# Kernel tuning notes

Hardware: AMD Instinct MI355X
Metric: run time of the kernel (lower is better)

## Reference

```python
import jax, jax.numpy as jnp
import numpy as np

TOP_K = 8
N_EXPERTS = 64
ALPHA = 0.1
NORM_TOPK = True
SEQ_AUX = True


def setup_inputs() -> dict:
    key = jax.random.key(0)
    k1, k2 = jax.random.split(key)
    B, S, H = 4, 4096, 2048
    hidden_states = jax.random.normal(k1, (B, S, H), dtype=jnp.float32)
    # kaiming_uniform_(a=sqrt(5)) => bound = 1/sqrt(fan_in)
    bound = 1.0 / np.sqrt(H)
    weight = jax.random.uniform(k2, (N_EXPERTS, H), dtype=jnp.float32,
                                minval=-bound, maxval=bound)
    return {"hidden_states": hidden_states, "weight": weight}


def reference(hidden_states, weight):
    B, S, H = hidden_states.shape
    E, K = N_EXPERTS, TOP_K
    x = hidden_states.reshape(-1, H)                 # [T, H], T = B*S
    logits = jnp.einsum('th,eh->te', x, weight)      # gating GEMM
    scores = jax.nn.softmax(logits, axis=-1)         # [T, E]
    topk_weight, topk_idx = jax.lax.top_k(scores, K) # [T, K]
    if K > 1 and NORM_TOPK:
        topk_weight = topk_weight / (topk_weight.sum(-1, keepdims=True) + 1e-20)

    # batch-level load stats (bincount over selections)
    expert_loads = jnp.zeros((E,), jnp.float32).at[topk_idx.reshape(-1)].add(1.0)

    # sequence-level auxiliary load-balancing loss
    if SEQ_AUX:
        idx_b = topk_idx.reshape(B, S * K)           # [B, S*K]
        ce = jnp.zeros((B, E), jnp.float32)
        ce = ce.at[jnp.arange(B)[:, None], idx_b].add(1.0)
        ce = ce / (S * K / E)
        mean_scores = scores.reshape(B, S, E).mean(axis=1)   # [B, E]
        aux_loss = (ce * mean_scores).sum(axis=1).mean() * ALPHA
    else:
        ce = jax.nn.one_hot(topk_idx.reshape(-1), E).mean(0)
        Pi = scores.mean(0)
        aux_loss = (Pi * ce * E).sum() * ALPHA

    return (topk_idx, topk_weight, aux_loss, expert_loads)
```

## Files before the change

### kernel.cpp

```cpp
#include <hip/hip_runtime.h>
#include <hip/hip_bf16.h>
#include <math.h>

#define TOK 16384
#define HDIM 2048
#define NE 64
#define NB 4
#define KTOP 8
#define KC 64
#define NC (HDIM / KC)

typedef __attribute__((ext_vector_type(8))) __bf16 bf16x8;
typedef __attribute__((ext_vector_type(4))) float f32x4;
typedef unsigned int uint;

__device__ __forceinline__ uint asu(float f) { union { float f; uint u; } c; c.f = f; return c.u; }
__device__ __forceinline__ float asf(uint u) { union { uint u; float f; } c; c.u = u; return c.f; }

__device__ __forceinline__ void split3(float v, uint& h, uint& m, uint& l) {
  uint u = asu(v);
  h = u & 0xffff0000u;
  float d = v - asf(h);
  m = asu(d) & 0xffff0000u;
  float d2 = d - asf(m);
  l = asu(d2);
}

__device__ __forceinline__ void split8(float4 a, float4 b,
                                       bf16x8& h8, bf16x8& m8, bf16x8& l8) {
  union { uint4 u; bf16x8 v; } H, M, L;
  uint h0, m0, l0, h1, m1, l1;
  split3(a.x, h0, m0, l0); split3(a.y, h1, m1, l1);
  H.u.x = (h0 >> 16) | (h1 & 0xffff0000u);
  M.u.x = (m0 >> 16) | (m1 & 0xffff0000u);
  L.u.x = (l0 >> 16) | (l1 & 0xffff0000u);
  split3(a.z, h0, m0, l0); split3(a.w, h1, m1, l1);
  H.u.y = (h0 >> 16) | (h1 & 0xffff0000u);
  M.u.y = (m0 >> 16) | (m1 & 0xffff0000u);
  L.u.y = (l0 >> 16) | (l1 & 0xffff0000u);
  split3(b.x, h0, m0, l0); split3(b.y, h1, m1, l1);
  H.u.z = (h0 >> 16) | (h1 & 0xffff0000u);
  M.u.z = (m0 >> 16) | (m1 & 0xffff0000u);
  L.u.z = (l0 >> 16) | (l1 & 0xffff0000u);
  split3(b.z, h0, m0, l0); split3(b.w, h1, m1, l1);
  H.u.w = (h0 >> 16) | (h1 & 0xffff0000u);
  M.u.w = (m0 >> 16) | (m1 & 0xffff0000u);
  L.u.w = (l0 >> 16) | (l1 & 0xffff0000u);
  h8 = H.v; m8 = M.v; l8 = L.v;
}

__device__ __forceinline__ void gl_lds16(const void* g, void* l) {
  __builtin_amdgcn_global_load_lds(
      (const __attribute__((address_space(1))) void*)g,
      (__attribute__((address_space(3))) void*)l, 16, 0, 0);
}

__global__ __launch_bounds__(256) void wsplit(const float* __restrict__ w,
                                              char* __restrict__ wpk) {
  int t = blockIdx.x * 256 + threadIdx.x;
  int lane = t & 63;
  int f2 = (t >> 6) & 1, half = (t >> 7) & 1, ks = (t >> 8) & 1, c = t >> 9;
  int e = half * 32 + f2 * 16 + (lane & 15);
  int k = c * 64 + ks * 32 + ((lane >> 4) << 3);
  const float* p = w + (size_t)e * HDIM + k;
  bf16x8 h8, m8, l8;
  split8(*(const float4*)p, *(const float4*)(p + 4), h8, m8, l8);
  union { bf16x8 v; uint4 u; } H, M, L;
  H.v = h8; M.v = m8; L.v = l8;
  size_t base = ((size_t)c * 24 + (size_t)(((ks * 2 + half) * 2 + f2) * 3)) * 1024
                + (size_t)lane * 16;
  *(uint4*)(wpk + base) = H.u;
  *(uint4*)(wpk + base + 1024) = M.u;
  *(uint4*)(wpk + base + 2048) = L.u;
}

__global__ __launch_bounds__(512) void gate_fused(const float* __restrict__ x,
                                                  const char* __restrict__ wpk,
                                                  float* __restrict__ out,
                                                  float* __restrict__ ce,
                                                  float* __restrict__ ssum) {
  __shared__ __align__(16) char lds[49152];
  __shared__ float hist[NE];

  const int tid = threadIdx.x;
  const int bid = blockIdx.x;
  const int t0 = bid * 64;
  const int b = bid >> 6;
  const int lane = tid & 63;
  const int wid = tid >> 6;
  const int half = wid & 1;
  const int tg = (wid >> 1) << 4;

  if (tid < NE) hist[tid] = 0.f;

  char* buf0 = lds;
  char* buf1 = lds + 24576;

  const float* xrow = x + (size_t)(t0 + tg + (lane & 15)) * HDIM + ((lane >> 4) << 3);

  f32x4 acc[2] = {{0.f, 0.f, 0.f, 0.f}, {0.f, 0.f, 0.f, 0.f}};

  {
    const char* wsp0 = wpk + (size_t)lane * 16;
    gl_lds16(wsp0 + (0 * 8 + wid) * 1024, buf0 + (0 * 8 + wid) * 1024);
    gl_lds16(wsp0 + (1 * 8 + wid) * 1024, buf0 + (1 * 8 + wid) * 1024);
    gl_lds16(wsp0 + (2 * 8 + wid) * 1024, buf0 + (2 * 8 + wid) * 1024);
  }
  float4 xa0 = *(const float4*)(xrow);
  float4 xa1 = *(const float4*)(xrow + 4);
  float4 xa2 = *(const float4*)(xrow + 32);
  float4 xa3 = *(const float4*)(xrow + 36);
  float4 xb0 = *(const float4*)(xrow + 64);
  float4 xb1 = *(const float4*)(xrow + 68);
  float4 xb2 = *(const float4*)(xrow + 96);
  float4 xb3 = *(const float4*)(xrow + 100);
  asm volatile("s_waitcnt vmcnt(4)" ::: "memory");
  __builtin_amdgcn_s_barrier();
  asm volatile("" ::: "memory");

#define CHUNK(c, X0, X1, X2, X3, BR, BW)                                        \
  {                                                                             \
    if ((c) + 1 < NC) {                              \
      const char* wsp = wpk + (size_t)((c) + 1) * 24576 + (size_t)lane * 16;    \
      gl_lds16(wsp + (0 * 8 + wid) * 1024, BW + (0 * 8 + wid) * 1024);          \
      gl_lds16(wsp + (1 * 8 + wid) * 1024, BW + (1 * 8 + wid) * 1024);          \
      gl_lds16(wsp + (2 * 8 + wid) * 1024, BW + (2 * 8 + wid) * 1024);          \
    }                                                                           \
    bf16x8 ah0, am0, al0, ah1, am1, al1;                     \
    split8(X0, X1, ah0, am0, al0);                                              \
    split8(X2, X3, ah1, am1, al1);                                              \
    if ((c) + 2 < NC) {                                    \
      const float* xp = xrow + ((c) + 2) * 64;                                  \
      X0 = *(const float4*)(xp);                                                \
      X1 = *(const float4*)(xp + 4);                                            \
      X2 = *(const float4*)(xp + 32);                                           \
      X3 = *(const float4*)(xp + 36);                                           \
    }                                                                           \
    _Pragma("unroll")                                 \
    for (int f2 = 0; f2 < 2; ++f2) {                                            \
      const char* bb0 = BR + (size_t)(((0 * 2 + half) * 2 + f2) * 3) * 1024 + lane * 16; \
      bf16x8 bh = *(const bf16x8*)(bb0);                                        \
      bf16x8 bm = *(const bf16x8*)(bb0 + 1024);                                 \
      bf16x8 bl = *(const bf16x8*)(bb0 + 2048);                                 \
      acc[f2] = __builtin_amdgcn_mfma_f32_16x16x32_bf16(ah0, bh, acc[f2], 0, 0, 0); \
      acc[f2] = __builtin_amdgcn_mfma_f32_16x16x32_bf16(ah0, bm, acc[f2], 0, 0, 0); \
      acc[f2] = __builtin_amdgcn_mfma_f32_16x16x32_bf16(am0, bh, acc[f2], 0, 0, 0); \
      acc[f2] = __builtin_amdgcn_mfma_f32_16x16x32_bf16(ah0, bl, acc[f2], 0, 0, 0); \
      acc[f2] = __builtin_amdgcn_mfma_f32_16x16x32_bf16(al0, bh, acc[f2], 0, 0, 0); \
      acc[f2] = __builtin_amdgcn_mfma_f32_16x16x32_bf16(am0, bm, acc[f2], 0, 0, 0); \
      const char* bb1 = BR + (size_t)(((1 * 2 + half) * 2 + f2) * 3) * 1024 + lane * 16; \
      bf16x8 kh = *(const bf16x8*)(bb1);                                        \
      bf16x8 km = *(const bf16x8*)(bb1 + 1024);                                 \
      bf16x8 kl = *(const bf16x8*)(bb1 + 2048);                                 \
      acc[f2] = __builtin_amdgcn_mfma_f32_16x16x32_bf16(ah1, kh, acc[f2], 0, 0, 0); \
      acc[f2] = __builtin_amdgcn_mfma_f32_16x16x32_bf16(ah1, km, acc[f2], 0, 0, 0); \
      acc[f2] = __builtin_amdgcn_mfma_f32_16x16x32_bf16(am1, kh, acc[f2], 0, 0, 0); \
      acc[f2] = __builtin_amdgcn_mfma_f32_16x16x32_bf16(ah1, kl, acc[f2], 0, 0, 0); \
      acc[f2] = __builtin_amdgcn_mfma_f32_16x16x32_bf16(al1, kh, acc[f2], 0, 0, 0); \
      acc[f2] = __builtin_amdgcn_mfma_f32_16x16x32_bf16(am1, km, acc[f2], 0, 0, 0); \
    }                                                                           \
          \
    if ((c) < NC - 2) { asm volatile("s_waitcnt vmcnt(4)" ::: "memory"); }      \
    else              { asm volatile("s_waitcnt vmcnt(0)" ::: "memory"); }      \
    __builtin_amdgcn_s_barrier();                                               \
    asm volatile("" ::: "memory");                                              \
  }

#pragma unroll 1
  for (int cc = 0; cc < NC; cc += 2) {
    CHUNK(cc,     xa0, xa1, xa2, xa3, buf0, buf1);
    CHUNK(cc + 1, xb0, xb1, xb2, xb3, buf1, buf0);
  }
#undef CHUNK

  float (*sc)[65] = (float(*)[65])lds;
#pragma unroll
  for (int f2 = 0; f2 < 2; ++f2) {
    int e = half * 32 + f2 * 16 + (lane & 15);
    int tk = tg + ((lane >> 4) << 2);
    sc[e][tk + 0] = acc[f2][0];
    sc[e][tk + 1] = acc[f2][1];
    sc[e][tk + 2] = acc[f2][2];
    sc[e][tk + 3] = acc[f2][3];
  }
  __syncthreads();

  const int t = tid >> 3;
  const int j = tid & 7;
  float p[8];
#pragma unroll
  for (int i = 0; i < 8; ++i) p[i] = sc[j * 8 + i][t];

  float m = p[0];
#pragma unroll
  for (int i = 1; i < 8; ++i) m = fmaxf(m, p[i]);
  m = fmaxf(m, __shfl_xor(m, 1, 8));
  m = fmaxf(m, __shfl_xor(m, 2, 8));
  m = fmaxf(m, __shfl_xor(m, 4, 8));
  float s = 0.f;
#pragma unroll
  for (int i = 0; i < 8; ++i) { p[i] = __expf(p[i] - m); s += p[i]; }
  s += __shfl_xor(s, 1, 8);
  s += __shfl_xor(s, 2, 8);
  s += __shfl_xor(s, 4, 8);
  float inv = 1.f / s;
#pragma unroll
  for (int i = 0; i < 8; ++i) { p[i] *= inv; sc[j * 8 + i][t] = p[i]; }

  unsigned used = 0;
  float wsum = 0.f;
  float wv[KTOP];
  int wi_[KTOP];
#pragma unroll
  for (int sel = 0; sel < KTOP; ++sel) {
    float bv = -1.f;
    int bi = 0;
#pragma unroll
    for (int i = 0; i < 8; ++i) {
      bool ok = !((used >> i) & 1u);
      if (ok && p[i] > bv) { bv = p[i]; bi = i; }
    }
    int ge = j * 8 + bi;
#pragma unroll
    for (int mk = 1; mk < 8; mk <<= 1) {
      float ov = __shfl_xor(bv, mk, 8);
      int og = __shfl_xor(ge, mk, 8);
      if (ov > bv || (ov == bv && og < ge)) { bv = ov; ge = og; }
    }
    if ((ge >> 3) == j) used |= 1u << (ge & 7);
    wv[sel] = bv;
    wi_[sel] = ge;
    wsum += bv;
  }
  if (j == 0) {
    float winv = 1.f / (wsum + 1e-20f);
#pragma unroll
    for (int sel = 0; sel < KTOP; ++sel) {
      out[(size_t)(t0 + t) * KTOP + sel] = (float)wi_[sel];
      out[(size_t)TOK * KTOP + (size_t)(t0 + t) * KTOP + sel] = wv[sel] * winv;
      atomicAdd(&hist[wi_[sel]], 1.f);
    }
  }
  __syncthreads();

  if (tid < NE) {
    float ssl = 0.f;
#pragma unroll
    for (int tt = 0; tt < 64; ++tt) ssl += sc[tid][tt];
    atomicAdd(&ssum[b * NE + tid], ssl);
    atomicAdd(&ce[b * NE + tid], hist[tid]);
  }
}

__global__ __launch_bounds__(64) void gate_final(const float* __restrict__ ce,
                                                 const float* __restrict__ ssum,
                                                 float* __restrict__ out) {
  const int e = threadIdx.x;
  float loads = 0.f, aux = 0.f;
#pragma unroll
  for (int b = 0; b < NB; ++b) {
    float c = ce[b * 64 + e];
    loads += c;
    aux += (c / 512.0f) * (ssum[b * 64 + e] / 4096.0f);
  }
  out[(size_t)2 * TOK * KTOP + 1 + e] = loads;
#pragma unroll
  for (int off = 32; off > 0; off >>= 1) aux += __shfl_down(aux, off);
  if (e == 0) out[(size_t)2 * TOK * KTOP] = aux * (0.1f / 4.0f);
}

extern "C" void kernel_launch(void* const* d_in, const int* in_sizes, int n_in,
                              void* d_out, int out_size, void* d_ws, size_t ws_size,
                              hipStream_t stream) {
  const float* x = (const float*)d_in[0];
  const float* w = (const float*)d_in[1];
  float* out = (float*)d_out;

  char* wpk = (char*)d_ws;
  float* ce = (float*)(wpk + (size_t)NC * 24576);
  float* ssum = ce + NB * NE;

  hipMemsetAsync(ce, 0, 2 * NB * NE * sizeof(float), stream);
  wsplit<<<dim3(64), dim3(256), 0, stream>>>(w, wpk);
  gate_fused<<<dim3(TOK / 64), dim3(512), 0, stream>>>(x, wpk, out, ce, ssum);
  gate_final<<<dim3(1), dim3(64), 0, stream>>>(ce, ssum, out);
}
```

Baseline: 60.72 us.

## Load packed weights straight to registers instead of staging through LDS

The GEMM main loop no longer stages the split bf16 weight chunks into double-buffered LDS with global_load_lds. Each wave now loads only its own half of the weights directly from global memory into register double buffers (WA/WB). This frees about 48KB of LDS and adds launch_bounds(512,2), which allows two blocks per CU. The hipMemsetAsync is folded into the wsplit kernel, and the explicit vmcnt waits are dropped. The costs are more register pressure from 24 uint4 buffers and redundant weight reads from L2 across the four token-group waves.

```diff
diff --git a/kernel.cpp b/kernel.cpp
--- a/kernel.cpp
+++ b/kernel.cpp
@@ -16,6 +16,7 @@
 
 __device__ __forceinline__ uint asu(float f) { union { float f; uint u; } c; c.f = f; return c.u; }
 __device__ __forceinline__ float asf(uint u) { union { uint u; float f; } c; c.u = u; return c.f; }
+__device__ __forceinline__ bf16x8 u2b(uint4 u) { union { uint4 u; bf16x8 b; } c; c.u = u; return c.b; }
 
 __device__ __forceinline__ void split3(float v, uint& h, uint& m, uint& l) {
   uint u = asu(v);
@@ -49,14 +50,12 @@
   h8 = H.v; m8 = M.v; l8 = L.v;
 }
 
-__device__ __forceinline__ void gl_lds16(const void* g, void* l) {
-  __builtin_amdgcn_global_load_lds(
-      (const __attribute__((address_space(1))) void*)g,
-      (__attribute__((address_space(3))) void*)l, 16, 0, 0);
-}
-
 __global__ __launch_bounds__(256) void wsplit(const float* __restrict__ w,
-                                              char* __restrict__ wpk) {
+                                              char* __restrict__ wpk,
+                                              float* __restrict__ stats) {
+  if (blockIdx.x == 0 && threadIdx.x < 128) {
+    *(float4*)(stats + threadIdx.x * 4) = make_float4(0.f, 0.f, 0.f, 0.f);
+  }
   int t = blockIdx.x * 256 + threadIdx.x;
   int lane = t & 63;
   int f2 = (t >> 6) & 1, half = (t >> 7) & 1, ks = (t >> 8) & 1, c = t >> 9;
@@ -67,19 +66,19 @@
   split8(*(const float4*)p, *(const float4*)(p + 4), h8, m8, l8);
   union { bf16x8 v; uint4 u; } H, M, L;
   H.v = h8; M.v = m8; L.v = l8;
-  size_t base = ((size_t)c * 24 + (size_t)(((ks * 2 + half) * 2 + f2) * 3)) * 1024
-                + (size_t)lane * 16;
+  size_t base = (size_t)c * 24576 + (size_t)ks * 12288 + (size_t)half * 6144
+              + (size_t)f2 * 3072 + (size_t)lane * 16;
   *(uint4*)(wpk + base) = H.u;
   *(uint4*)(wpk + base + 1024) = M.u;
   *(uint4*)(wpk + base + 2048) = L.u;
 }
 
-__global__ __launch_bounds__(512) void gate_fused(const float* __restrict__ x,
-                                                  const char* __restrict__ wpk,
-                                                  float* __restrict__ out,
-                                                  float* __restrict__ ce,
-                                                  float* __restrict__ ssum) {
-  __shared__ __align__(16) char lds[49152];
+__global__ __launch_bounds__(512, 2) void gate_fused(const float* __restrict__ x,
+                                                     const char* __restrict__ wpk,
+                                                     float* __restrict__ out,
+                                                     float* __restrict__ ce,
+                                                     float* __restrict__ ssum) {
+  __shared__ float sc[NE][65];
   __shared__ float hist[NE];
 
   const int tid = threadIdx.x;
@@ -93,87 +92,79 @@
 
   if (tid < NE) hist[tid] = 0.f;
 
-  char* buf0 = lds;
-  char* buf1 = lds + 24576;
-
   const float* xrow = x + (size_t)(t0 + tg + (lane & 15)) * HDIM + ((lane >> 4) << 3);
+  const char* wbase = wpk + half * 6144 + lane * 16;
 
   f32x4 acc[2] = {{0.f, 0.f, 0.f, 0.f}, {0.f, 0.f, 0.f, 0.f}};
-
-  {
-    const char* wsp0 = wpk + (size_t)lane * 16;
-    gl_lds16(wsp0 + (0 * 8 + wid) * 1024, buf0 + (0 * 8 + wid) * 1024);
-    gl_lds16(wsp0 + (1 * 8 + wid) * 1024, buf0 + (1 * 8 + wid) * 1024);
-    gl_lds16(wsp0 + (2 * 8 + wid) * 1024, buf0 + (2 * 8 + wid) * 1024);
-  }
-  float4 xa0 = *(const float4*)(xrow);
-  float4 xa1 = *(const float4*)(xrow + 4);
-  float4 xa2 = *(const float4*)(xrow + 32);
-  float4 xa3 = *(const float4*)(xrow + 36);
-  float4 xb0 = *(const float4*)(xrow + 64);
-  float4 xb1 = *(const float4*)(xrow + 68);
-  float4 xb2 = *(const float4*)(xrow + 96);
-  float4 xb3 = *(const float4*)(xrow + 100);
-  asm volatile("s_waitcnt vmcnt(4)" ::: "memory");
-  __builtin_amdgcn_s_barrier();
-  asm volatile("" ::: "memory");
-
-#define CHUNK(c, X0, X1, X2, X3, BR, BW)                                        \
-  {                                                                             \
-    if ((c) + 1 < NC) {                              \
-      const char* wsp = wpk + (size_t)((c) + 1) * 24576 + (size_t)lane * 16;    \
-      gl_lds16(wsp + (0 * 8 + wid) * 1024, BW + (0 * 8 + wid) * 1024);          \
-      gl_lds16(wsp + (1 * 8 + wid) * 1024, BW + (1 * 8 + wid) * 1024);          \
-      gl_lds16(wsp + (2 * 8 + wid) * 1024, BW + (2 * 8 + wid) * 1024);          \
-    }                                                                           \
-    bf16x8 ah0, am0, al0, ah1, am1, al1;                     \
-    split8(X0, X1, ah0, am0, al0);                                              \
-    split8(X2, X3, ah1, am1, al1);                                              \
-    if ((c) + 2 < NC) {                                    \
-      const float* xp = xrow + ((c) + 2) * 64;                                  \
-      X0 = *(const float4*)(xp);                                                \
-      X1 = *(const float4*)(xp + 4);                                            \
-      X2 = *(const float4*)(xp + 32);                                           \
-      X3 = *(const float4*)(xp + 36);                                           \
-    }                                                                           \
-    _Pragma("unroll")                                 \
-    for (int f2 = 0; f2 < 2; ++f2) {                                            \
-      const char* bb0 = BR + (size_t)(((0 * 2 + half) * 2 + f2) * 3) * 1024 + lane * 16; \
-      bf16x8 bh = *(const bf16x8*)(bb0);                                        \
-      bf16x8 bm = *(const bf16x8*)(bb0 + 1024);                                 \
-      bf16x8 bl = *(const bf16x8*)(bb0 + 2048);                                 \
-      acc[f2] = __builtin_amdgcn_mfma_f32_16x16x32_bf16(ah0, bh, acc[f2], 0, 0, 0); \
-      acc[f2] = __builtin_amdgcn_mfma_f32_16x16x32_bf16(ah0, bm, acc[f2], 0, 0, 0); \
-      acc[f2] = __builtin_amdgcn_mfma_f32_16x16x32_bf16(am0, bh, acc[f2], 0, 0, 0); \
-      acc[f2] = __builtin_amdgcn_mfma_f32_16x16x32_bf16(ah0, bl, acc[f2], 0, 0, 0); \
-      acc[f2] = __builtin_amdgcn_mfma_f32_16x16x32_bf16(al0, bh, acc[f2], 0, 0, 0); \
-      acc[f2] = __builtin_amdgcn_mfma_f32_16x16x32_bf16(am0, bm, acc[f2], 0, 0, 0); \
-      const char* bb1 = BR + (size_t)(((1 * 2 + half) * 2 + f2) * 3) * 1024 + lane * 16; \
-      bf16x8 kh = *(const bf16x8*)(bb1);                                        \
-      bf16x8 km = *(const bf16x8*)(bb1 + 1024);                                 \
-      bf16x8 kl = *(const bf16x8*)(bb1 + 2048);                                 \
-      acc[f2] = __builtin_amdgcn_mfma_f32_16x16x32_bf16(ah1, kh, acc[f2], 0, 0, 0); \
-      acc[f2] = __builtin_amdgcn_mfma_f32_16x16x32_bf16(ah1, km, acc[f2], 0, 0, 0); \
-      acc[f2] = __builtin_amdgcn_mfma_f32_16x16x32_bf16(am1, kh, acc[f2], 0, 0, 0); \
-      acc[f2] = __builtin_amdgcn_mfma_f32_16x16x32_bf16(ah1, kl, acc[f2], 0, 0, 0); \
-      acc[f2] = __builtin_amdgcn_mfma_f32_16x16x32_bf16(al1, kh, acc[f2], 0, 0, 0); \
-      acc[f2] = __builtin_amdgcn_mfma_f32_16x16x32_bf16(am1, km, acc[f2], 0, 0, 0); \
-    }                                                                           \
-          \
-    if ((c) < NC - 2) { asm volatile("s_waitcnt vmcnt(4)" ::: "memory"); }      \
-    else              { asm volatile("s_waitcnt vmcnt(0)" ::: "memory"); }      \
-    __builtin_amdgcn_s_barrier();                                               \
-    asm volatile("" ::: "memory");                                              \
-  }
+  uint4 WA[12], WB[12];
+  float4 xa0, xa1, xa2, xa3, xb0, xb1, xb2, xb3;
+
+#define LOADW(W, c)                                                           \
+  {                                                                           \
+    const char* wp_ = wbase + (size_t)(c) * 24576;                            \
+    _Pragma("unroll")                                                         \
+    for (int ks = 0; ks < 2; ++ks)                                            \
+      _Pragma("unroll")                                                       \
+      for (int f2 = 0; f2 < 2; ++f2)                                          \
+        _Pragma("unroll")                                                     \
+        for (int pl = 0; pl < 3; ++pl)                                        \
+          W[ks * 6 + f2 * 3 + pl] =                                           \
+              *(const uint4*)(wp_ + ks * 12288 + f2 * 3072 + pl * 1024);      \
+  }
+
+#define LOADX(V0, V1, V2, V3, c)                                              \
+  {                                                                           \
+    const float* xp_ = xrow + (size_t)(c) * 64;                               \
+    V0 = *(const float4*)(xp_);                                               \
+    V1 = *(const float4*)(xp_ + 4);                                           \
+    V2 = *(const float4*)(xp_ + 32);                                          \
+    V3 = *(const float4*)(xp_ + 36);                                          \
+  }
+
+#define BODY(W, WN, X0, X1, X2, X3, c)                                        \
+  {                                                                           \
+    if ((c) + 1 < NC) LOADW(WN, (c) + 1);                                     \
+    bf16x8 ah0, am0, al0, ah1, am1, al1;                                      \
+    split8(X0, X1, ah0, am0, al0);                                            \
+    split8(X2, X3, ah1, am1, al1);                                            \
+    if ((c) + 2 < NC) LOADX(X0, X1, X2, X3, (c) + 2);                         \
+    _Pragma("unroll")                                                         \
+    for (int f2 = 0; f2 < 2; ++f2) {                                          \
+      bf16x8 bh0 = u2b(W[f2 * 3 + 0]);                                        \
+      bf16x8 bm0 = u2b(W[f2 * 3 + 1]);                                        \
+      bf16x8 bl0 = u2b(W[f2 * 3 + 2]);                                        \
+      acc[f2] = __builtin_amdgcn_mfma_f32_16x16x32_bf16(ah0, bh0, acc[f2], 0, 0, 0); \
+      acc[f2] = __builtin_amdgcn_mfma_f32_16x16x32_bf16(ah0, bm0, acc[f2], 0, 0, 0); \
+      acc[f2] = __builtin_amdgcn_mfma_f32_16x16x32_bf16(am0, bh0, acc[f2], 0, 0, 0); \
+      acc[f2] = __builtin_amdgcn_mfma_f32_16x16x32_bf16(ah0, bl0, acc[f2], 0, 0, 0); \
+      acc[f2] = __builtin_amdgcn_mfma_f32_16x16x32_bf16(al0, bh0, acc[f2], 0, 0, 0); \
+      acc[f2] = __builtin_amdgcn_mfma_f32_16x16x32_bf16(am0, bm0, acc[f2], 0, 0, 0); \
+      bf16x8 bh1 = u2b(W[6 + f2 * 3 + 0]);                                    \
+      bf16x8 bm1 = u2b(W[6 + f2 * 3 + 1]);                                    \
+      bf16x8 bl1 = u2b(W[6 + f2 * 3 + 2]);                                    \
+      acc[f2] = __builtin_amdgcn_mfma_f32_16x16x32_bf16(ah1, bh1, acc[f2], 0, 0, 0); \
+      acc[f2] = __builtin_amdgcn_mfma_f32_16x16x32_bf16(ah1, bm1, acc[f2], 0, 0, 0); \
+      acc[f2] = __builtin_amdgcn_mfma_f32_16x16x32_bf16(am1, bh1, acc[f2], 0, 0, 0); \
+      acc[f2] = __builtin_amdgcn_mfma_f32_16x16x32_bf16(ah1, bl1, acc[f2], 0, 0, 0); \
+      acc[f2] = __builtin_amdgcn_mfma_f32_16x16x32_bf16(al1, bh1, acc[f2], 0, 0, 0); \
+      acc[f2] = __builtin_amdgcn_mfma_f32_16x16x32_bf16(am1, bm1, acc[f2], 0, 0, 0); \
+    }                                                                         \
+    __builtin_amdgcn_s_barrier();             \
+  }
+
+  LOADW(WA, 0);
+  LOADX(xa0, xa1, xa2, xa3, 0);
+  LOADX(xb0, xb1, xb2, xb3, 1);
 
 #pragma unroll 1
   for (int cc = 0; cc < NC; cc += 2) {
-    CHUNK(cc,     xa0, xa1, xa2, xa3, buf0, buf1);
-    CHUNK(cc + 1, xb0, xb1, xb2, xb3, buf1, buf0);
-  }
-#undef CHUNK
-
-  float (*sc)[65] = (float(*)[65])lds;
+    BODY(WA, WB, xa0, xa1, xa2, xa3, cc);
+    BODY(WB, WA, xb0, xb1, xb2, xb3, cc + 1);
+  }
+#undef BODY
+#undef LOADW
+#undef LOADX
+
 #pragma unroll
   for (int f2 = 0; f2 < 2; ++f2) {
     int e = half * 32 + f2 * 16 + (lane & 15);
@@ -280,8 +271,7 @@
   float* ce = (float*)(wpk + (size_t)NC * 24576);
   float* ssum = ce + NB * NE;
 
-  hipMemsetAsync(ce, 0, 2 * NB * NE * sizeof(float), stream);
-  wsplit<<<dim3(64), dim3(256), 0, stream>>>(w, wpk);
+  wsplit<<<dim3(64), dim3(256), 0, stream>>>(w, wpk, ce);
   gate_fused<<<dim3(TOK / 64), dim3(512), 0, stream>>>(x, wpk, out, ce, ssum);
   gate_final<<<dim3(1), dim3(64), 0, stream>>>(ce, ssum, out);
 }
```

Measured after the change: 73.52 us. +21.1%, slower.

## Halve gating block tile to 32 tokens and fold stats zeroing into wsplit

Applied to the files above, without the earlier changes.

The fused gating kernel now processes 32 tokens per block with 256 threads instead of 64 tokens with 512, doubling the grid and allowing two blocks per CU. Each wave now issues six 16-byte global-to-LDS loads per weight chunk instead of three, and the scratch-score stride and wait counts are adjusted to match. The separate memset of the load and score statistics is removed; the first wsplit block zeroes them instead, saving one launch. In exchange, every packed weight chunk is streamed from L2 twice as many times overall, and the per-block reduction and global atomics are doubled.

```diff
diff --git a/kernel.cpp b/kernel.cpp
--- a/kernel.cpp
+++ b/kernel.cpp
@@ -9,6 +9,7 @@
 #define KTOP 8
 #define KC 64
 #define NC (HDIM / KC)
+#define BT 32
 
 typedef __attribute__((ext_vector_type(8))) __bf16 bf16x8;
 typedef __attribute__((ext_vector_type(4))) float f32x4;
@@ -56,7 +57,11 @@
 }
 
 __global__ __launch_bounds__(256) void wsplit(const float* __restrict__ w,
-                                              char* __restrict__ wpk) {
+                                              char* __restrict__ wpk,
+                                              float* __restrict__ stats) {
+  if (blockIdx.x == 0 && threadIdx.x < 128) {
+    *(float4*)(stats + threadIdx.x * 4) = make_float4(0.f, 0.f, 0.f, 0.f);
+  }
   int t = blockIdx.x * 256 + threadIdx.x;
   int lane = t & 63;
   int f2 = (t >> 6) & 1, half = (t >> 7) & 1, ks = (t >> 8) & 1, c = t >> 9;
@@ -67,25 +72,25 @@
   split8(*(const float4*)p, *(const float4*)(p + 4), h8, m8, l8);
   union { bf16x8 v; uint4 u; } H, M, L;
   H.v = h8; M.v = m8; L.v = l8;
-  size_t base = ((size_t)c * 24 + (size_t)(((ks * 2 + half) * 2 + f2) * 3)) * 1024
-                + (size_t)lane * 16;
+  size_t base = (size_t)c * 24576 + (size_t)ks * 12288 + (size_t)half * 6144
+              + (size_t)f2 * 3072 + (size_t)lane * 16;
   *(uint4*)(wpk + base) = H.u;
   *(uint4*)(wpk + base + 1024) = M.u;
   *(uint4*)(wpk + base + 2048) = L.u;
 }
 
-__global__ __launch_bounds__(512) void gate_fused(const float* __restrict__ x,
-                                                  const char* __restrict__ wpk,
-                                                  float* __restrict__ out,
-                                                  float* __restrict__ ce,
-                                                  float* __restrict__ ssum) {
+__global__ __launch_bounds__(256, 2) void gate_fused(const float* __restrict__ x,
+                                                     const char* __restrict__ wpk,
+                                                     float* __restrict__ out,
+                                                     float* __restrict__ ce,
+                                                     float* __restrict__ ssum) {
   __shared__ __align__(16) char lds[49152];
   __shared__ float hist[NE];
 
   const int tid = threadIdx.x;
   const int bid = blockIdx.x;
-  const int t0 = bid * 64;
-  const int b = bid >> 6;
+  const int t0 = bid * BT;
+  const int b = bid >> 7;
   const int lane = tid & 63;
   const int wid = tid >> 6;
   const int half = wid & 1;
@@ -102,9 +107,9 @@
 
   {
     const char* wsp0 = wpk + (size_t)lane * 16;
-    gl_lds16(wsp0 + (0 * 8 + wid) * 1024, buf0 + (0 * 8 + wid) * 1024);
-    gl_lds16(wsp0 + (1 * 8 + wid) * 1024, buf0 + (1 * 8 + wid) * 1024);
-    gl_lds16(wsp0 + (2 * 8 + wid) * 1024, buf0 + (2 * 8 + wid) * 1024);
+#pragma unroll
+    for (int i = 0; i < 6; ++i)
+      gl_lds16(wsp0 + (i * 4 + wid) * 1024, buf0 + (i * 4 + wid) * 1024);
   }
   float4 xa0 = *(const float4*)(xrow);
   float4 xa1 = *(const float4*)(xrow + 4);
@@ -114,23 +119,23 @@
   float4 xb1 = *(const float4*)(xrow + 68);
   float4 xb2 = *(const float4*)(xrow + 96);
   float4 xb3 = *(const float4*)(xrow + 100);
-  asm volatile("s_waitcnt vmcnt(4)" ::: "memory");
+  asm volatile("s_waitcnt vmcnt(8)" ::: "memory");
   __builtin_amdgcn_s_barrier();
   asm volatile("" ::: "memory");
 
 #define CHUNK(c, X0, X1, X2, X3, BR, BW)                                        \
   {                                                                             \
-    if ((c) + 1 < NC) {                              \
+    if ((c) + 1 < NC) {          \
       const char* wsp = wpk + (size_t)((c) + 1) * 24576 + (size_t)lane * 16;    \
-      gl_lds16(wsp + (0 * 8 + wid) * 1024, BW + (0 * 8 + wid) * 1024);          \
-      gl_lds16(wsp + (1 * 8 + wid) * 1024, BW + (1 * 8 + wid) * 1024);          \
-      gl_lds16(wsp + (2 * 8 + wid) * 1024, BW + (2 * 8 + wid) * 1024);          \
+      _Pragma("unroll")                                                         \
+      for (int i = 0; i < 6; ++i)                                               \
+        gl_lds16(wsp + (i * 4 + wid) * 1024, BW + (i * 4 + wid) * 1024);        \
     }                                                                           \
     bf16x8 ah0, am0, al0, ah1, am1, al1;                     \
     split8(X0, X1, ah0, am0, al0);                                              \
     split8(X2, X3, ah1, am1, al1);                                              \
     if ((c) + 2 < NC) {                                    \
-      const float* xp = xrow + ((c) + 2) * 64;                                  \
+      const float* xp = xrow + (size_t)((c) + 2) * 64;                          \
       X0 = *(const float4*)(xp);                                                \
       X1 = *(const float4*)(xp + 4);                                            \
       X2 = *(const float4*)(xp + 32);                                           \
@@ -138,7 +143,7 @@
     }                                                                           \
     _Pragma("unroll")                                 \
     for (int f2 = 0; f2 < 2; ++f2) {                                            \
-      const char* bb0 = BR + (size_t)(((0 * 2 + half) * 2 + f2) * 3) * 1024 + lane * 16; \
+      const char* bb0 = BR + half * 6144 + f2 * 3072 + lane * 16;               \
       bf16x8 bh = *(const bf16x8*)(bb0);                                        \
       bf16x8 bm = *(const bf16x8*)(bb0 + 1024);                                 \
       bf16x8 bl = *(const bf16x8*)(bb0 + 2048);                                 \
@@ -148,7 +153,7 @@
       acc[f2] = __builtin_amdgcn_mfma_f32_16x16x32_bf16(ah0, bl, acc[f2], 0, 0, 0); \
       acc[f2] = __builtin_amdgcn_mfma_f32_16x16x32_bf16(al0, bh, acc[f2], 0, 0, 0); \
       acc[f2] = __builtin_amdgcn_mfma_f32_16x16x32_bf16(am0, bm, acc[f2], 0, 0, 0); \
-      const char* bb1 = BR + (size_t)(((1 * 2 + half) * 2 + f2) * 3) * 1024 + lane * 16; \
+      const char* bb1 = BR + 12288 + half * 6144 + f2 * 3072 + lane * 16;       \
       bf16x8 kh = *(const bf16x8*)(bb1);                                        \
       bf16x8 km = *(const bf16x8*)(bb1 + 1024);                                 \
       bf16x8 kl = *(const bf16x8*)(bb1 + 2048);                                 \
@@ -173,7 +178,7 @@
   }
 #undef CHUNK
 
-  float (*sc)[65] = (float(*)[65])lds;
+  float (*sc)[33] = (float(*)[33])lds;
 #pragma unroll
   for (int f2 = 0; f2 < 2; ++f2) {
     int e = half * 32 + f2 * 16 + (lane & 15);
@@ -246,7 +251,7 @@
   if (tid < NE) {
     float ssl = 0.f;
 #pragma unroll
-    for (int tt = 0; tt < 64; ++tt) ssl += sc[tid][tt];
+    for (int tt = 0; tt < BT; ++tt) ssl += sc[tid][tt];
     atomicAdd(&ssum[b * NE + tid], ssl);
     atomicAdd(&ce[b * NE + tid], hist[tid]);
   }
@@ -280,8 +285,7 @@
   float* ce = (float*)(wpk + (size_t)NC * 24576);
   float* ssum = ce + NB * NE;
 
-  hipMemsetAsync(ce, 0, 2 * NB * NE * sizeof(float), stream);
-  wsplit<<<dim3(64), dim3(256), 0, stream>>>(w, wpk);
-  gate_fused<<<dim3(TOK / 64), dim3(512), 0, stream>>>(x, wpk, out, ce, ssum);
+  wsplit<<<dim3(64), dim3(256), 0, stream>>>(w, wpk, ce);
+  gate_fused<<<dim3(TOK / BT), dim3(256), 0, stream>>>(x, wpk, out, ce, ssum);
   gate_final<<<dim3(1), dim3(64), 0, stream>>>(ce, ssum, out);
 }
```

After: 66.28 us. +9.2%, slower.
